# Kernel optimization log

Measured on AMD Instinct MI355X. Metric: run time of the kernel, lower is better.

## Reference

```python
import jax, jax.numpy as jnp
import numpy as np

B, S, D = 64, 8192, 64

def setup_inputs() -> dict:
    key = jax.random.key(0)
    kq, kk, kv = jax.random.split(key, 3)
    q = jax.random.normal(kq, (B, S, D), dtype=jnp.float32)
    k = jax.random.normal(kk, (B, S, D), dtype=jnp.float32)
    v = jax.random.normal(kv, (B, S, D), dtype=jnp.float32)
    return {"q": q, "k": k, "v": v}

def _feature_map(x):
    # ELU(x) + 1
    return jax.nn.elu(x) + 1.0

def reference(q, k, v):
    qf = _feature_map(q)              # [B, S, D]
    kf = _feature_map(k)              # [B, S, D]
    k_sum = kf.sum(axis=-2)           # [B, D]
    kv = jnp.einsum('bsd,bse->bde', kf, v)        # [B, D, D]
    deno = jnp.maximum(jnp.einsum('bsd,bd->bs', qf, k_sum), 1e-4)  # [B, S]
    o = jnp.einsum('bsd,bde->bse', qf, kv) / deno[..., None]       # [B, S, D]
    return o
```

## Files before the change

### kernel.cpp

```cpp
#include <hip/hip_runtime.h>
#include <math.h>

#define BB 64
#define SS 8192
#define DD 64

constexpr int C1 = 8;
constexpr int CHUNK1 = SS / C1;
constexpr int C2 = 16;
constexpr int CHUNK2 = SS / C2;

__device__ __forceinline__ float fmap(float x) {
    return x > 0.0f ? x + 1.0f : __expf(x);
}

__global__ __launch_bounds__(256) void phase1_kernel(
    const float* __restrict__ k,
    const float* __restrict__ v,
    float* __restrict__ kv_ws,
    float* __restrict__ ksum_ws)
{
    __shared__ float Ks[64 * 64];
    __shared__ float Vs[64 * 64];

    const int t = threadIdx.x;
    const int b = blockIdx.y;
    const int s_chunk0 = blockIdx.x * CHUNK1;
    const int dgrp = t >> 4;
    const int egrp = t & 15;
    const int d0 = dgrp * 4;
    const int e0 = egrp * 4;

    const float* kb = k + (size_t)b * SS * DD;
    const float* vb = v + (size_t)b * SS * DD;

    float acc[4][4] = {};
    float ks_acc[4] = {};

    for (int tile = 0; tile < CHUNK1 / 64; ++tile) {
        const int s_base = s_chunk0 + tile * 64;
        __syncthreads();
        #pragma unroll
        for (int i = 0; i < 4; ++i) {
            const int idx = t + i * 256;
            const int row = idx >> 4;
            const int c4  = idx & 15;
            const size_t goff = (size_t)(s_base + row) * DD + c4 * 4;
            float4 kk = *(const float4*)(kb + goff);
            kk.x = fmap(kk.x); kk.y = fmap(kk.y);
            kk.z = fmap(kk.z); kk.w = fmap(kk.w);
            *(float4*)(Ks + row * 64 + c4 * 4) = kk;
            float4 vv = *(const float4*)(vb + goff);
            *(float4*)(Vs + row * 64 + c4 * 4) = vv;
        }
        __syncthreads();
        #pragma unroll 4
        for (int s = 0; s < 64; ++s) {
            float4 kf4 = *(const float4*)(Ks + s * 64 + d0);
            float4 vv4 = *(const float4*)(Vs + s * 64 + e0);
            const float kf[4] = {kf4.x, kf4.y, kf4.z, kf4.w};
            const float vvv[4] = {vv4.x, vv4.y, vv4.z, vv4.w};
            #pragma unroll
            for (int i = 0; i < 4; ++i) {
                #pragma unroll
                for (int j = 0; j < 4; ++j) acc[i][j] += kf[i] * vvv[j];
                ks_acc[i] += kf[i];
            }
        }
    }

    float* kvb = kv_ws + (size_t)b * DD * DD;
    #pragma unroll
    for (int i = 0; i < 4; ++i) {
        #pragma unroll
        for (int j = 0; j < 4; ++j) {
            atomicAdd(kvb + (d0 + i) * DD + e0 + j, acc[i][j]);
        }
    }
    if (egrp == 0) {
        #pragma unroll
        for (int i = 0; i < 4; ++i) {
            atomicAdd(ksum_ws + b * DD + d0 + i, ks_acc[i]);
        }
    }
}

__global__ __launch_bounds__(256) void phase2_kernel(
    const float* __restrict__ q,
    const float* __restrict__ kv_ws,
    const float* __restrict__ ksum_ws,
    float* __restrict__ o)
{
    __shared__ float kvS[64 * 64];
    __shared__ float ksS[64];
    __shared__ float qS[64 * 68];

    const int t = threadIdx.x;
    const int b = blockIdx.y;
    const int s_chunk0 = blockIdx.x * CHUNK2;
    const int sgrp = t >> 4;
    const int egrp = t & 15;
    const int s0 = sgrp * 4;
    const int e0 = egrp * 4;

    {
        const float4* kvb = (const float4*)(kv_ws + (size_t)b * DD * DD);
        #pragma unroll
        for (int i = 0; i < 4; ++i) {
            const int idx = t + i * 256;
            ((float4*)kvS)[idx] = kvb[idx];
        }
        if (t < 16) ((float4*)ksS)[t] = ((const float4*)(ksum_ws + b * DD))[t];
    }

    const float* qb = q + (size_t)b * SS * DD;
    float*       ob = o + (size_t)b * SS * DD;

    for (int tile = 0; tile < CHUNK2 / 64; ++tile) {
        const int s_base = s_chunk0 + tile * 64;
        __syncthreads();
        #pragma unroll
        for (int i = 0; i < 4; ++i) {
            const int idx = t + i * 256;
            const int row = idx >> 4;
            const int c4  = idx & 15;
            float4 qq = *(const float4*)(qb + (size_t)(s_base + row) * DD + c4 * 4);
            qq.x = fmap(qq.x); qq.y = fmap(qq.y);
            qq.z = fmap(qq.z); qq.w = fmap(qq.w);
            *(float4*)(qS + row * 68 + c4 * 4) = qq;
        }
        __syncthreads();

        float acc[4][4] = {};
        float dacc[4] = {};
        #pragma unroll 4
        for (int dc = 0; dc < 16; ++dc) {
            float4 kst = *(const float4*)(ksS + dc * 4);
            const float ks4[4] = {kst.x, kst.y, kst.z, kst.w};
            float qv[4][4];
            #pragma unroll
            for (int sr = 0; sr < 4; ++sr) {
                float4 x = *(const float4*)(qS + (s0 + sr) * 68 + dc * 4);
                qv[sr][0] = x.x; qv[sr][1] = x.y; qv[sr][2] = x.z; qv[sr][3] = x.w;
            }
            #pragma unroll
            for (int dj = 0; dj < 4; ++dj) {
                float4 kv4 = *(const float4*)(kvS + (dc * 4 + dj) * 64 + e0);
                const float kvr[4] = {kv4.x, kv4.y, kv4.z, kv4.w};
                #pragma unroll
                for (int sr = 0; sr < 4; ++sr) {
                    const float qq = qv[sr][dj];
                    acc[sr][0] += qq * kvr[0];
                    acc[sr][1] += qq * kvr[1];
                    acc[sr][2] += qq * kvr[2];
                    acc[sr][3] += qq * kvr[3];
                    dacc[sr]   += qq * ks4[dj];
                }
            }
        }
        #pragma unroll
        for (int sr = 0; sr < 4; ++sr) {
            const float r = 1.0f / fmaxf(dacc[sr], 1e-4f);
            float4 outv;
            outv.x = acc[sr][0] * r;
            outv.y = acc[sr][1] * r;
            outv.z = acc[sr][2] * r;
            outv.w = acc[sr][3] * r;
            *(float4*)(ob + (size_t)(s_base + s0 + sr) * DD + e0) = outv;
        }
    }
}

extern "C" void kernel_launch(void* const* d_in, const int* in_sizes, int n_in,
                              void* d_out, int out_size, void* d_ws, size_t ws_size,
                              hipStream_t stream) {
    const float* q = (const float*)d_in[0];
    const float* k = (const float*)d_in[1];
    const float* v = (const float*)d_in[2];
    float* o = (float*)d_out;

    float* kv_ws   = (float*)d_ws;
    float* ksum_ws = kv_ws + (size_t)BB * DD * DD;
    const size_t ws_bytes = ((size_t)BB * DD * DD + (size_t)BB * DD) * sizeof(float);

    hipMemsetAsync(d_ws, 0, ws_bytes, stream);

    dim3 g1(C1, BB), g2(C2, BB), blk(256);
    phase1_kernel<<<g1, blk, 0, stream>>>(k, v, kv_ws, ksum_ws);
    phase2_kernel<<<g2, blk, 0, stream>>>(q, kv_ws, ksum_ws, o);
}
```

Before: 464.8 us.

## Use bf16 MFMA for output projection and double-buffer phase-1 KV accumulation

Phase 2 now keeps a transposed KV matrix in registers as bf16 fragments and computes q·KV with 16x16x32 bf16 MFMA instructions per wavefront, reading q straight from global memory with no shared-memory staging. Phase 1 double-buffers the K/V tiles with a register prefetch, gives each thread an 8x8 register tile, and adds the four wavefronts' partial sums in shared memory before one set of atomics. These changes aim to cut FMA issue cost, atomic traffic and load stalls, but bf16 rounding of q and KV adds numerical error. Output stores are scalar and strided, which may reduce write efficiency.

```diff
diff --git a/kernel.cpp b/kernel.cpp
--- a/kernel.cpp
+++ b/kernel.cpp
@@ -7,166 +7,258 @@
 
 constexpr int C1 = 8;
 constexpr int CHUNK1 = SS / C1;
-constexpr int C2 = 16;
-constexpr int CHUNK2 = SS / C2;
+constexpr int TILES1 = CHUNK1 / 64;
+
+typedef __attribute__((ext_vector_type(8))) short bf16x8;
+typedef __attribute__((ext_vector_type(4))) float f32x4;
 
 __device__ __forceinline__ float fmap(float x) {
     return x > 0.0f ? x + 1.0f : __expf(x);
+}
+
+__device__ __forceinline__ short f2bf(float x) {
+    unsigned int u = __float_as_uint(x);
+    u += 0x7FFFu + ((u >> 16) & 1u);
+    return (short)(u >> 16);
 }
 
 __global__ __launch_bounds__(256) void phase1_kernel(
     const float* __restrict__ k,
     const float* __restrict__ v,
-    float* __restrict__ kv_ws,
+    float* __restrict__ kvT_ws,
     float* __restrict__ ksum_ws)
 {
-    __shared__ float Ks[64 * 64];
-    __shared__ float Vs[64 * 64];
-
-    const int t = threadIdx.x;
-    const int b = blockIdx.y;
-    const int s_chunk0 = blockIdx.x * CHUNK1;
-    const int dgrp = t >> 4;
-    const int egrp = t & 15;
-    const int d0 = dgrp * 4;
-    const int e0 = egrp * 4;
+    __shared__ float Ks[2][64 * 64];
+    __shared__ float Vs[2][64 * 64];
+
+    const int t    = threadIdx.x;
+    const int lane = t & 63;
+    const int w    = t >> 6;
+    const int b    = blockIdx.y;
+    const int schunk = blockIdx.x * CHUNK1;
 
     const float* kb = k + (size_t)b * SS * DD;
     const float* vb = v + (size_t)b * SS * DD;
 
-    float acc[4][4] = {};
-    float ks_acc[4] = {};
-
-    for (int tile = 0; tile < CHUNK1 / 64; ++tile) {
-        const int s_base = s_chunk0 + tile * 64;
-        __syncthreads();
+    const int d0  = (lane >> 3) * 8;
+    const int e0  = (lane & 7) * 8;
+    const int sw0 = w * 16;
+
+    float acc[8][8] = {};
+    float ksa[8] = {};
+
+    {
+        const float* kt = kb + (size_t)schunk * DD;
+        const float* vt = vb + (size_t)schunk * DD;
         #pragma unroll
         for (int i = 0; i < 4; ++i) {
-            const int idx = t + i * 256;
-            const int row = idx >> 4;
-            const int c4  = idx & 15;
-            const size_t goff = (size_t)(s_base + row) * DD + c4 * 4;
-            float4 kk = *(const float4*)(kb + goff);
+            const int idx = (t + i * 256) * 4;
+            float4 kk = *(const float4*)(kt + idx);
+            float4 vv = *(const float4*)(vt + idx);
             kk.x = fmap(kk.x); kk.y = fmap(kk.y);
             kk.z = fmap(kk.z); kk.w = fmap(kk.w);
-            *(float4*)(Ks + row * 64 + c4 * 4) = kk;
-            float4 vv = *(const float4*)(vb + goff);
-            *(float4*)(Vs + row * 64 + c4 * 4) = vv;
+            *(float4*)(&Ks[0][idx]) = kk;
+            *(float4*)(&Vs[0][idx]) = vv;
+        }
+    }
+    __syncthreads();
+
+    for (int tile = 0; tile < TILES1; ++tile) {
+        const int cur = tile & 1;
+        float4 kreg[4], vreg[4];
+        const bool pf = (tile < TILES1 - 1);
+        if (pf) {
+            const float* kt = kb + (size_t)(schunk + (tile + 1) * 64) * DD;
+            const float* vt = vb + (size_t)(schunk + (tile + 1) * 64) * DD;
+            #pragma unroll
+            for (int i = 0; i < 4; ++i) {
+                const int idx = (t + i * 256) * 4;
+                kreg[i] = *(const float4*)(kt + idx);
+                vreg[i] = *(const float4*)(vt + idx);
+            }
+        }
+        const float* Kc = Ks[cur];
+        const float* Vc = Vs[cur];
+        #pragma unroll 4
+        for (int s = 0; s < 16; ++s) {
+            const float* krow = Kc + (sw0 + s) * 64;
+            const float* vrow = Vc + (sw0 + s) * 64;
+            float4 k0 = *(const float4*)(krow + d0);
+            float4 k1 = *(const float4*)(krow + d0 + 4);
+            float4 v0 = *(const float4*)(vrow + e0);
+            float4 v1 = *(const float4*)(vrow + e0 + 4);
+            const float kf[8] = {k0.x,k0.y,k0.z,k0.w,k1.x,k1.y,k1.z,k1.w};
+            const float vv[8] = {v0.x,v0.y,v0.z,v0.w,v1.x,v1.y,v1.z,v1.w};
+            #pragma unroll
+            for (int i = 0; i < 8; ++i) {
+                ksa[i] += kf[i];
+                #pragma unroll
+                for (int j = 0; j < 8; ++j) acc[i][j] += kf[i] * vv[j];
+            }
+        }
+        if (pf) {
+            float* Kn = Ks[cur ^ 1];
+            float* Vn = Vs[cur ^ 1];
+            #pragma unroll
+            for (int i = 0; i < 4; ++i) {
+                const int idx = (t + i * 256) * 4;
+                float4 kk = kreg[i];
+                kk.x = fmap(kk.x); kk.y = fmap(kk.y);
+                kk.z = fmap(kk.z); kk.w = fmap(kk.w);
+                *(float4*)(&Kn[idx]) = kk;
+                *(float4*)(&Vn[idx]) = vreg[i];
+            }
         }
         __syncthreads();
-        #pragma unroll 4
-        for (int s = 0; s < 64; ++s) {
-            float4 kf4 = *(const float4*)(Ks + s * 64 + d0);
-            float4 vv4 = *(const float4*)(Vs + s * 64 + e0);
-            const float kf[4] = {kf4.x, kf4.y, kf4.z, kf4.w};
-            const float vvv[4] = {vv4.x, vv4.y, vv4.z, vv4.w};
-            #pragma unroll
-            for (int i = 0; i < 4; ++i) {
-                #pragma unroll
-                for (int j = 0; j < 4; ++j) acc[i][j] += kf[i] * vvv[j];
-                ks_acc[i] += kf[i];
-            }
-        }
-    }
-
-    float* kvb = kv_ws + (size_t)b * DD * DD;
-    #pragma unroll
-    for (int i = 0; i < 4; ++i) {
-        #pragma unroll
-        for (int j = 0; j < 4; ++j) {
-            atomicAdd(kvb + (d0 + i) * DD + e0 + j, acc[i][j]);
-        }
-    }
-    if (egrp == 0) {
-        #pragma unroll
-        for (int i = 0; i < 4; ++i) {
-            atomicAdd(ksum_ws + b * DD + d0 + i, ks_acc[i]);
-        }
+    }
+
+    if ((lane & 7) == 0) {
+        #pragma unroll
+        for (int i = 0; i < 8; ++i)
+            atomicAdd(ksum_ws + b * DD + d0 + i, ksa[i]);
+    }
+
+    float* scr0 = &Ks[0][0];
+    float* scr1 = &Vs[0][0];
+    if (w & 1) {
+        float* dst = (w == 1) ? scr0 : scr1;
+        #pragma unroll
+        for (int i = 0; i < 8; ++i)
+            #pragma unroll
+            for (int jj = 0; jj < 2; ++jj)
+                *(float4*)(dst + (i * 2 + jj) * 256 + lane * 4) =
+                    make_float4(acc[i][jj*4], acc[i][jj*4+1], acc[i][jj*4+2], acc[i][jj*4+3]);
+    }
+    __syncthreads();
+    if (!(w & 1)) {
+        const float* src = (w == 0) ? scr0 : scr1;
+        #pragma unroll
+        for (int i = 0; i < 8; ++i)
+            #pragma unroll
+            for (int jj = 0; jj < 2; ++jj) {
+                float4 x = *(const float4*)(src + (i * 2 + jj) * 256 + lane * 4);
+                acc[i][jj*4]   += x.x;
+                acc[i][jj*4+1] += x.y;
+                acc[i][jj*4+2] += x.z;
+                acc[i][jj*4+3] += x.w;
+            }
+    }
+    __syncthreads();
+    if (w == 2) {
+        #pragma unroll
+        for (int i = 0; i < 8; ++i)
+            #pragma unroll
+            for (int jj = 0; jj < 2; ++jj)
+                *(float4*)(scr0 + (i * 2 + jj) * 256 + lane * 4) =
+                    make_float4(acc[i][jj*4], acc[i][jj*4+1], acc[i][jj*4+2], acc[i][jj*4+3]);
+    }
+    __syncthreads();
+    if (w == 0) {
+        #pragma unroll
+        for (int i = 0; i < 8; ++i)
+            #pragma unroll
+            for (int jj = 0; jj < 2; ++jj) {
+                float4 x = *(const float4*)(scr0 + (i * 2 + jj) * 256 + lane * 4);
+                acc[i][jj*4]   += x.x;
+                acc[i][jj*4+1] += x.y;
+                acc[i][jj*4+2] += x.z;
+                acc[i][jj*4+3] += x.w;
+            }
+        float* kvb = kvT_ws + (size_t)b * DD * DD;
+        #pragma unroll
+        for (int i = 0; i < 8; ++i)
+            #pragma unroll
+            for (int j = 0; j < 8; ++j)
+                atomicAdd(kvb + (e0 + j) * DD + (d0 + i), acc[i][j]);
     }
 }
 
 __global__ __launch_bounds__(256) void phase2_kernel(
     const float* __restrict__ q,
-    const float* __restrict__ kv_ws,
+    const float* __restrict__ kvT_ws,
     const float* __restrict__ ksum_ws,
     float* __restrict__ o)
 {
-    __shared__ float kvS[64 * 64];
-    __shared__ float ksS[64];
-    __shared__ float qS[64 * 68];
-
-    const int t = threadIdx.x;
-    const int b = blockIdx.y;
-    const int s_chunk0 = blockIdx.x * CHUNK2;
-    const int sgrp = t >> 4;
-    const int egrp = t & 15;
-    const int s0 = sgrp * 4;
-    const int e0 = egrp * 4;
-
-    {
-        const float4* kvb = (const float4*)(kv_ws + (size_t)b * DD * DD);
-        #pragma unroll
-        for (int i = 0; i < 4; ++i) {
-            const int idx = t + i * 256;
-            ((float4*)kvS)[idx] = kvb[idx];
-        }
-        if (t < 16) ((float4*)ksS)[t] = ((const float4*)(ksum_ws + b * DD))[t];
+    const int t    = threadIdx.x;
+    const int lane = t & 63;
+    const int w    = t >> 6;
+    const int b    = blockIdx.y;
+    const int wid  = blockIdx.x * 4 + w;
+    const int g    = lane >> 4;
+    const int c    = lane & 15;
+
+    const float* kvb = kvT_ws + (size_t)b * DD * DD;
+    bf16x8 Bfrag[4][2];
+    #pragma unroll
+    for (int et = 0; et < 4; ++et) {
+        #pragma unroll
+        for (int dk = 0; dk < 2; ++dk) {
+            const float* p = kvb + (et * 16 + c) * DD + dk * 32 + g * 8;
+            float4 lo = *(const float4*)p;
+            float4 hi = *(const float4*)(p + 4);
+            bf16x8 f;
+            f[0] = f2bf(lo.x); f[1] = f2bf(lo.y); f[2] = f2bf(lo.z); f[3] = f2bf(lo.w);
+            f[4] = f2bf(hi.x); f[5] = f2bf(hi.y); f[6] = f2bf(hi.z); f[7] = f2bf(hi.w);
+            Bfrag[et][dk] = f;
+        }
+    }
+    float ksr[16];
+    #pragma unroll
+    for (int dk = 0; dk < 2; ++dk) {
+        const float* p = ksum_ws + b * DD + dk * 32 + g * 8;
+        float4 lo = *(const float4*)p;
+        float4 hi = *(const float4*)(p + 4);
+        ksr[dk*8+0] = lo.x; ksr[dk*8+1] = lo.y; ksr[dk*8+2] = lo.z; ksr[dk*8+3] = lo.w;
+        ksr[dk*8+4] = hi.x; ksr[dk*8+5] = hi.y; ksr[dk*8+6] = hi.z; ksr[dk*8+7] = hi.w;
     }
 
     const float* qb = q + (size_t)b * SS * DD;
     float*       ob = o + (size_t)b * SS * DD;
 
-    for (int tile = 0; tile < CHUNK2 / 64; ++tile) {
-        const int s_base = s_chunk0 + tile * 64;
-        __syncthreads();
-        #pragma unroll
-        for (int i = 0; i < 4; ++i) {
-            const int idx = t + i * 256;
-            const int row = idx >> 4;
-            const int c4  = idx & 15;
-            float4 qq = *(const float4*)(qb + (size_t)(s_base + row) * DD + c4 * 4);
-            qq.x = fmap(qq.x); qq.y = fmap(qq.y);
-            qq.z = fmap(qq.z); qq.w = fmap(qq.w);
-            *(float4*)(qS + row * 68 + c4 * 4) = qq;
-        }
-        __syncthreads();
-
-        float acc[4][4] = {};
-        float dacc[4] = {};
-        #pragma unroll 4
-        for (int dc = 0; dc < 16; ++dc) {
-            float4 kst = *(const float4*)(ksS + dc * 4);
-            const float ks4[4] = {kst.x, kst.y, kst.z, kst.w};
-            float qv[4][4];
-            #pragma unroll
-            for (int sr = 0; sr < 4; ++sr) {
-                float4 x = *(const float4*)(qS + (s0 + sr) * 68 + dc * 4);
-                qv[sr][0] = x.x; qv[sr][1] = x.y; qv[sr][2] = x.z; qv[sr][3] = x.w;
-            }
-            #pragma unroll
-            for (int dj = 0; dj < 4; ++dj) {
-                float4 kv4 = *(const float4*)(kvS + (dc * 4 + dj) * 64 + e0);
-                const float kvr[4] = {kv4.x, kv4.y, kv4.z, kv4.w};
-                #pragma unroll
-                for (int sr = 0; sr < 4; ++sr) {
-                    const float qq = qv[sr][dj];
-                    acc[sr][0] += qq * kvr[0];
-                    acc[sr][1] += qq * kvr[1];
-                    acc[sr][2] += qq * kvr[2];
-                    acc[sr][3] += qq * kvr[3];
-                    dacc[sr]   += qq * ks4[dj];
-                }
-            }
-        }
-        #pragma unroll
-        for (int sr = 0; sr < 4; ++sr) {
-            const float r = 1.0f / fmaxf(dacc[sr], 1e-4f);
-            float4 outv;
-            outv.x = acc[sr][0] * r;
-            outv.y = acc[sr][1] * r;
-            outv.z = acc[sr][2] * r;
-            outv.w = acc[sr][3] * r;
-            *(float4*)(ob + (size_t)(s_base + s0 + sr) * DD + e0) = outv;
+    #pragma unroll 1
+    for (int tt = 0; tt < 8; ++tt) {
+        const int s0 = wid * 128 + tt * 16;
+        const float* qrow = qb + (size_t)(s0 + c) * DD;
+        float qf[16];
+        #pragma unroll
+        for (int dk = 0; dk < 2; ++dk) {
+            float4 lo = *(const float4*)(qrow + dk * 32 + g * 8);
+            float4 hi = *(const float4*)(qrow + dk * 32 + g * 8 + 4);
+            qf[dk*8+0] = fmap(lo.x); qf[dk*8+1] = fmap(lo.y);
+            qf[dk*8+2] = fmap(lo.z); qf[dk*8+3] = fmap(lo.w);
+            qf[dk*8+4] = fmap(hi.x); qf[dk*8+5] = fmap(hi.y);
+            qf[dk*8+6] = fmap(hi.z); qf[dk*8+7] = fmap(hi.w);
+        }
+        float dn = 0.0f;
+        #pragma unroll
+        for (int i = 0; i < 16; ++i) dn += qf[i] * ksr[i];
+        dn += __shfl_xor(dn, 16, 64);
+        dn += __shfl_xor(dn, 32, 64);
+
+        bf16x8 A0, A1;
+        #pragma unroll
+        for (int i = 0; i < 8; ++i) { A0[i] = f2bf(qf[i]); A1[i] = f2bf(qf[8+i]); }
+
+        f32x4 acc0 = {0.f,0.f,0.f,0.f}, acc1 = {0.f,0.f,0.f,0.f};
+        f32x4 acc2 = {0.f,0.f,0.f,0.f}, acc3 = {0.f,0.f,0.f,0.f};
+        acc0 = __builtin_amdgcn_mfma_f32_16x16x32_bf16(A0, Bfrag[0][0], acc0, 0, 0, 0);
+        acc0 = __builtin_amdgcn_mfma_f32_16x16x32_bf16(A1, Bfrag[0][1], acc0, 0, 0, 0);
+        acc1 = __builtin_amdgcn_mfma_f32_16x16x32_bf16(A0, Bfrag[1][0], acc1, 0, 0, 0);
+        acc1 = __builtin_amdgcn_mfma_f32_16x16x32_bf16(A1, Bfrag[1][1], acc1, 0, 0, 0);
+        acc2 = __builtin_amdgcn_mfma_f32_16x16x32_bf16(A0, Bfrag[2][0], acc2, 0, 0, 0);
+        acc2 = __builtin_amdgcn_mfma_f32_16x16x32_bf16(A1, Bfrag[2][1], acc2, 0, 0, 0);
+        acc3 = __builtin_amdgcn_mfma_f32_16x16x32_bf16(A0, Bfrag[3][0], acc3, 0, 0, 0);
+        acc3 = __builtin_amdgcn_mfma_f32_16x16x32_bf16(A1, Bfrag[3][1], acc3, 0, 0, 0);
+
+        #pragma unroll
+        for (int r = 0; r < 4; ++r) {
+            float dr  = __shfl(dn, (g << 2) + r, 64);
+            float inv = 1.0f / fmaxf(dr, 1e-4f);
+            float* op = ob + (size_t)(s0 + (g << 2) + r) * DD + c;
+            op[0]  = acc0[r] * inv;
+            op[16] = acc1[r] * inv;
+            op[32] = acc2[r] * inv;
+            op[48] = acc3[r] * inv;
         }
     }
 }
@@ -179,13 +271,13 @@
     const float* v = (const float*)d_in[2];
     float* o = (float*)d_out;
 
-    float* kv_ws   = (float*)d_ws;
-    float* ksum_ws = kv_ws + (size_t)BB * DD * DD;
+    float* kvT_ws  = (float*)d_ws;
+    float* ksum_ws = kvT_ws + (size_t)BB * DD * DD;
     const size_t ws_bytes = ((size_t)BB * DD * DD + (size_t)BB * DD) * sizeof(float);
 
     hipMemsetAsync(d_ws, 0, ws_bytes, stream);
 
-    dim3 g1(C1, BB), g2(C2, BB), blk(256);
-    phase1_kernel<<<g1, blk, 0, stream>>>(k, v, kv_ws, ksum_ws);
-    phase2_kernel<<<g2, blk, 0, stream>>>(q, kv_ws, ksum_ws, o);
-}
+    dim3 g1(C1, BB), g2(16, BB), blk(256);
+    phase1_kernel<<<g1, blk, 0, stream>>>(k, v, kvT_ws, ksum_ws);
+    phase2_kernel<<<g2, blk, 0, stream>>>(q, kvT_ws, ksum_ws, o);
+}
```

New measurement: 463.3 us. About the same (-0.3%).
